# Kernel tuning notes

Hardware: AMD Instinct MI355X
Metric: run time of the kernel (lower is better)

The kernel has to match this reference:

```python
import jax, jax.numpy as jnp
import numpy as np

D_MODEL = 1024
D_STATE = 16
D_CONV = 4
EXPAND = 2
D_INNER = EXPAND * D_MODEL
DT_RANK = (D_MODEL + 15) // 16  # 64
EPS = 1e-5


def dwconv(x, w, b, pad):
    # x: (B, C, L), w: (C, 1, K), depthwise conv
    y = jax.lax.conv_general_dilated(x, w, (1,), [pad],
                                     dimension_numbers=('NCH', 'OIH', 'NCH'),
                                     feature_group_count=x.shape[1])
    return y + b[None, :, None]


def mamba(x, W_inproj, m_conv_w, m_conv_b, W_xproj, W_dt, b_dt, A_log, Dp, W_outproj):
    # x: (B, L, d_model)
    Bn, L, _ = x.shape
    xz = x @ W_inproj.T                       # (B, L, 2*d_inner)
    xi, z = jnp.split(xz, 2, axis=-1)
    # causal depthwise conv: pad (K-1, 0) == torch pad K-1 then slice [:L]
    xc = dwconv(jnp.swapaxes(xi, 1, 2), m_conv_w, m_conv_b, (D_CONV - 1, 0))
    u = jax.nn.silu(jnp.swapaxes(xc, 1, 2))   # (B, L, d_inner)
    x_dbl = u @ W_xproj.T                     # (B, L, dt_rank + 2*d_state)
    dt = x_dbl[..., :DT_RANK]
    Bm = x_dbl[..., DT_RANK:DT_RANK + D_STATE]
    Cm = x_dbl[..., DT_RANK + D_STATE:]
    dt = jax.nn.softplus(dt @ W_dt.T + b_dt)  # (B, L, d_inner)
    A = -jnp.exp(A_log)                       # (d_inner, d_state)

    def step(h, inp):
        dt_t, B_t, C_t, u_t = inp             # (B,di),(B,ds),(B,ds),(B,di)
        dA = jnp.exp(dt_t[..., None] * A)     # (B, di, ds)
        h = dA * h + dt_t[..., None] * B_t[:, None, :] * u_t[..., None]
        y = jnp.einsum('bds,bs->bd', h, C_t)
        return h, y

    tm = lambda a: jnp.swapaxes(a, 0, 1)      # time-major for scan
    h0 = jnp.zeros((Bn, D_INNER, D_STATE), x.dtype)
    _, ys = jax.lax.scan(step, h0, (tm(dt), tm(Bm), tm(Cm), tm(u)))
    y = jnp.swapaxes(ys, 0, 1) + u * Dp       # (B, L, d_inner)
    y = y * jax.nn.silu(z)
    return y @ W_outproj.T                    # (B, L, d_model)


def forward(x, ln_g, ln_b, W_in, b_in, conv_w, conv_b,
            W_inproj, m_conv_w, m_conv_b, W_xproj, W_dt, b_dt,
            A_log, Dp, W_outproj, W_out, b_out):
    h = jnp.swapaxes(x, 1, 2)                 # (B, L, d_model)
    mu = h.mean(-1, keepdims=True)
    var = ((h - mu) ** 2).mean(-1, keepdims=True)
    h = (h - mu) / jnp.sqrt(var + EPS) * ln_g + ln_b
    h = h @ W_in.T + b_in
    # outer depthwise conv: kernel 4, pad 2 each side -> length L+1 (faithful)
    h = dwconv(jnp.swapaxes(h, 1, 2), conv_w, conv_b, (D_CONV // 2, D_CONV // 2))
    h = jax.nn.silu(h)
    h = jnp.swapaxes(h, 1, 2)                 # (B, L+1, d_model)
    y = mamba(h, W_inproj, m_conv_w, m_conv_b, W_xproj, W_dt, b_dt, A_log, Dp, W_outproj)
    y = y @ W_out.T + b_out
    return jnp.swapaxes(y, 1, 2)              # (B, d_model, L+1)


def setup_inputs() -> dict:
    key = jax.random.key(0)
    ks = jax.random.split(key, 16)
    B, L = 2, 2048
    s = 0.02
    inp = {
        'x': jax.random.normal(ks[0], (B, D_MODEL, L), jnp.float32),
        'ln_g': jnp.ones((D_MODEL,), jnp.float32),
        'ln_b': jnp.zeros((D_MODEL,), jnp.float32),
        'W_in': jax.random.normal(ks[1], (D_MODEL, D_MODEL), jnp.float32) * s,
        'b_in': jnp.zeros((D_MODEL,), jnp.float32),
        'conv_w': jax.random.normal(ks[2], (D_MODEL, 1, D_CONV), jnp.float32) * 0.3,
        'conv_b': jnp.zeros((D_MODEL,), jnp.float32),
        'W_inproj': jax.random.normal(ks[3], (2 * D_INNER, D_MODEL), jnp.float32) * s,
        'm_conv_w': jax.random.normal(ks[4], (D_INNER, 1, D_CONV), jnp.float32) * 0.3,
        'm_conv_b': jnp.zeros((D_INNER,), jnp.float32),
        'W_xproj': jax.random.normal(ks[5], (DT_RANK + 2 * D_STATE, D_INNER), jnp.float32) * s,
        'W_dt': jax.random.normal(ks[6], (D_INNER, DT_RANK), jnp.float32) * (DT_RANK ** -0.5),
        'b_dt': jax.random.uniform(ks[7], (D_INNER,), jnp.float32, -4.6, -2.0),
        'A_log': jnp.log(jnp.tile(jnp.arange(1, D_STATE + 1, dtype=jnp.float32)[None, :], (D_INNER, 1))),
        'Dp': jnp.ones((D_INNER,), jnp.float32),
        'W_outproj': jax.random.normal(ks[8], (D_MODEL, D_INNER), jnp.float32) * s,
        'W_out': jax.random.normal(ks[9], (D_MODEL, D_MODEL), jnp.float32) * s,
        'b_out': jnp.zeros((D_MODEL,), jnp.float32),
    }
    return inp


def reference(x, ln_g, ln_b, W_in, b_in, conv_w, conv_b, W_inproj, m_conv_w, m_conv_b,
              W_xproj, W_dt, b_dt, A_log, Dp, W_outproj, W_out, b_out):
    return forward(x, ln_g, ln_b, W_in, b_in, conv_w, conv_b, W_inproj, m_conv_w,
                   m_conv_b, W_xproj, W_dt, b_dt, A_log, Dp, W_outproj, W_out, b_out)
```

## Files before the change

kernel.cpp:

```cpp
#include <hip/hip_runtime.h>
#include <hip/hip_bf16.h>

#define DMODEL 1024
#define DINNER 2048
#define DTRANK 64
#define NPROJ  96
#define BATCH  2
#define LIN    2048
#define LOUT   2049
#define MTOT0  4096
#define MTOT1  4098
#define TC     32
#define NCH    65

typedef __attribute__((ext_vector_type(8))) short short8;
typedef __attribute__((ext_vector_type(4))) float f32x4;

__device__ __forceinline__ float f_silu(float x)     { return x / (1.f + __expf(-x)); }
__device__ __forceinline__ float f_softplus(float x) { return (x > 20.f) ? x : log1pf(__expf(x)); }
__device__ __forceinline__ short f2b(float x)
{
    __hip_bfloat16 b = __float2bfloat16(x);
    return *reinterpret_cast<short*>(&b);
}
__device__ __forceinline__ void gload16(const void* g, void* l)
{
    __builtin_amdgcn_global_load_lds(
        (const __attribute__((address_space(1))) void*)g,
        (__attribute__((address_space(3))) void*)l,
        16, 0, 0);
}
__device__ __forceinline__ void xcd_swizzle(int& bx, int& by)
{
    int nx = gridDim.x;
    int nwg = nx * gridDim.y;
    int f = blockIdx.x + blockIdx.y * nx;
    int xcd = f & 7, i = f >> 3;
    int q = nwg >> 3, r = nwg & 7;
    int w = (xcd < r ? xcd * (q + 1) : r * (q + 1) + (xcd - r) * q) + i;
    bx = w % nx;
    by = w / nx;
}

__global__ void ln_stats_k(const float* __restrict__ x, float* __restrict__ mu, float* __restrict__ rs)
{
    int b  = blockIdx.y;
    int l0 = blockIdx.x * 64;
    int lc = threadIdx.x & 63;
    int q  = threadIdx.x >> 6;
    const float* xb = x + (size_t)b * DMODEL * LIN + (l0 + lc);
    float s = 0.f, ss = 0.f;
    for (int c = q * 256; c < q * 256 + 256; ++c) {
        float v = xb[(size_t)c * LIN];
        s += v; ss += v * v;
    }
    __shared__ float Ss[4][64];
    __shared__ float Sq[4][64];
    Ss[q][lc] = s; Sq[q][lc] = ss;
    __syncthreads();
    if (threadIdx.x < 64) {
        float st = Ss[0][lc] + Ss[1][lc] + Ss[2][lc] + Ss[3][lc];
        float sq = Sq[0][lc] + Sq[1][lc] + Sq[2][lc] + Sq[3][lc];
        float m = st * (1.f / DMODEL);
        float v = sq * (1.f / DMODEL) - m * m;
        mu[b * LIN + l0 + lc] = m;
        rs[b * LIN + l0 + lc] = 1.f / sqrtf(v + 1e-5f);
    }
}

__global__ void lnT_k(const float* __restrict__ x, const float* __restrict__ mu,
                      const float* __restrict__ rs, const float* __restrict__ g,
                      const float* __restrict__ be, short* __restrict__ h0T)
{
    __shared__ float T[32][33];
    int l0 = blockIdx.x * 32;
    int c0 = blockIdx.y * 32;
    int b  = blockIdx.z;
    int tx = threadIdx.x & 31, ty = threadIdx.x >> 5;
    const float* xb = x + ((size_t)b * DMODEL + c0) * LIN + l0;
#pragma unroll
    for (int i = 0; i < 4; i++) {
        int cl = ty + 8 * i;
        T[cl][tx] = xb[(size_t)cl * LIN + tx];
    }
    __syncthreads();
    int c = c0 + tx;
    float gg = g[c], bb = be[c];
#pragma unroll
    for (int i = 0; i < 4; i++) {
        int ll = ty + 8 * i;
        int m = b * LIN + l0 + ll;
        float v = (T[tx][ll] - mu[m]) * rs[m] * gg + bb;
        h0T[(size_t)m * DMODEL + c] = f2b(v);
    }
}

__global__ void wdtT_k(const float* __restrict__ W_dt, float* __restrict__ WdtT)
{
    __shared__ float T[32][33];
    int n0 = blockIdx.x * 32;
    int k0 = blockIdx.y * 32;
    int tx = threadIdx.x & 31, ty = threadIdx.x >> 5;
#pragma unroll
    for (int i = 0; i < 4; i++) {
        int r = ty + 8 * i;
        T[r][tx] = W_dt[(size_t)(n0 + r) * 64 + k0 + tx];
    }
    __syncthreads();
#pragma unroll
    for (int i = 0; i < 4; i++) {
        int r = ty + 8 * i;
        WdtT[(size_t)(k0 + r) * 2048 + n0 + tx] = T[tx][r];
    }
}

__global__ void cvt_all_k(const float* __restrict__ W_in, const float* __restrict__ W_inproj,
                          const float* __restrict__ W_xproj,
                          const float* __restrict__ W_outproj, const float* __restrict__ W_out,
                          short* __restrict__ Wib, short* __restrict__ Winpb,
                          short* __restrict__ Wxpb,
                          short* __restrict__ Wopb, short* __restrict__ Wob)
{
    int b = blockIdx.x;
    const float* s; short* d; int i;
    if      (b < 1024) { s = W_in;      d = Wib;   i = b; }
    else if (b < 5120) { s = W_inproj;  d = Winpb; i = b - 1024; }
    else if (b < 5312) { s = W_xproj;   d = Wxpb;  i = b - 5120; }
    else if (b < 7360) { s = W_outproj; d = Wopb;  i = b - 5312; }
    else               { s = W_out;     d = Wob;   i = b - 7360; }
    int idx = (i * 256 + threadIdx.x) * 4;
    float4 v = *(const float4*)(s + idx);
    d[idx + 0] = f2b(v.x); d[idx + 1] = f2b(v.y);
    d[idx + 2] = f2b(v.z); d[idx + 3] = f2b(v.w);
}

template<int EPI>
__global__ __launch_bounds__(256) void gemm_bf(
    const short* __restrict__ A, int lda,
    const short* __restrict__ W, int ldb,
    float* __restrict__ C, int ldc,
    short* __restrict__ Cb, int ldcb,
    int M, int N, int K,
    const float* __restrict__ bias)
{
    __shared__ char LDSall[16896];
    short* As = (short*)LDSall;
    short* Bs = (short*)(LDSall + 8192);

    int tid  = threadIdx.x;
    int lane = tid & 63, wid = tid >> 6;
    int wr = wid >> 1, wc = wid & 1;
    int fr = lane & 15, kg = lane >> 4;
    int bx, by;
    xcd_swizzle(bx, by);
    int m0 = bx * 128, n0 = by * 128;

    int scol  = (lane & 3) * 8;
    int srow0 = wid * 32 + (lane >> 2);
    int srow1 = srow0 + 16;
    const short* a0 = A + (size_t)(m0 + srow0) * lda + scol;
    const short* a1 = A + (size_t)(m0 + srow1) * lda + scol;
    const short* b0 = W + (size_t)(n0 + srow0) * ldb + scol;
    const short* b1 = W + (size_t)(n0 + srow1) * ldb + scol;
    char* asd0 = LDSall + (wid * 2 + 0) * 1024;
    char* asd1 = LDSall + (wid * 2 + 1) * 1024;
    char* bsd0 = LDSall + 8192 + (wid * 2 + 0) * 1024;
    char* bsd1 = LDSall + 8192 + (wid * 2 + 1) * 1024;

    f32x4 acc[4][4];
#pragma unroll
    for (int mi = 0; mi < 4; mi++)
#pragma unroll
        for (int ni = 0; ni < 4; ni++) acc[mi][ni] = (f32x4){0.f, 0.f, 0.f, 0.f};

    for (int k0 = 0; k0 < K; k0 += 32) {
        gload16(a0 + k0, asd0);
        gload16(a1 + k0, asd1);
        gload16(b0 + k0, bsd0);
        gload16(b1 + k0, bsd1);
        __syncthreads();

        short8 af[4], bf[4];
#pragma unroll
        for (int mi = 0; mi < 4; mi++)
            af[mi] = *(const short8*)&As[(wr * 64 + mi * 16 + fr) * 32 + kg * 8];
#pragma unroll
        for (int ni = 0; ni < 4; ni++)
            bf[ni] = *(const short8*)&Bs[(wc * 64 + ni * 16 + fr) * 32 + kg * 8];
#pragma unroll
        for (int mi = 0; mi < 4; mi++)
#pragma unroll
            for (int ni = 0; ni < 4; ni++)
                acc[mi][ni] = __builtin_amdgcn_mfma_f32_16x16x32_bf16(
                    af[mi], bf[ni], acc[mi][ni], 0, 0, 0);
        __syncthreads();
    }

    float* ctile = (float*)LDSall;
    int row = tid >> 3;
    int cs  = (tid & 7) * 16;
#pragma unroll
    for (int p = 0; p < 4; p++) {
        __syncthreads();
#pragma unroll
        for (int ni = 0; ni < 4; ni++)
#pragma unroll
            for (int r = 0; r < 4; r++)
                ctile[(wr * 16 + kg * 4 + r) * 132 + wc * 64 + ni * 16 + fr] = acc[p][ni][r];
        __syncthreads();
        int mrow = m0 + ((row < 16) ? (p * 16 + row) : (64 + p * 16 + (row - 16)));
        int n = n0 + cs;
        if (mrow >= M || n >= N) continue;
        const float* src = &ctile[row * 132 + cs];
        if (EPI == 5) {
            float bv = bias[mrow];
            if (n + 15 < N && !(n < LOUT && n + 15 >= LOUT)) {
                int bq = (n >= LOUT) ? 1 : 0;
                float* dst = C + ((size_t)bq * DMODEL + mrow) * LOUT + (n - bq * LOUT);
#pragma unroll
                for (int e = 0; e < 4; e++) {
                    f32x4 v = *(const f32x4*)(src + 4 * e);
                    v += bv;
                    *(f32x4*)(dst + 4 * e) = v;
                }
            } else {
                for (int j = 0; j < 16; j++) {
                    int nj = n + j;
                    if (nj < N) {
                        int bq = (nj >= LOUT) ? 1 : 0;
                        C[((size_t)bq * DMODEL + mrow) * LOUT + (nj - bq * LOUT)] = src[j] + bv;
                    }
                }
            }
        } else if (EPI == 4) {
            short8 o0, o1;
#pragma unroll
            for (int e = 0; e < 8; e++) { o0[e] = f2b(src[e]); o1[e] = f2b(src[8 + e]); }
            *(short8*)&Cb[(size_t)mrow * ldcb + n]     = o0;
            *(short8*)&Cb[(size_t)mrow * ldcb + n + 8] = o1;
        } else {
#pragma unroll
            for (int e = 0; e < 4; e++) {
                f32x4 v = *(const f32x4*)(src + 4 * e);
                if (EPI == 1) v += *(const f32x4*)&bias[n + 4 * e];
                *(f32x4*)&C[(size_t)mrow * ldc + n + 4 * e] = v;
            }
        }
    }
}

__global__ __launch_bounds__(256) void dtfuse2_k(const float* __restrict__ xdbl,
                                                 const float* __restrict__ WdtT,
                                                 const float* __restrict__ b_dt,
                                                 float* __restrict__ dtout)
{
    int t  = threadIdx.x;
    int m0 = blockIdx.x * 8;
    __shared__ float dr[8][64];
    {
        int k = t & 63, r = t >> 6;
        int ma = m0 + r, mb = m0 + r + 4;
        dr[r][k]     = (ma < MTOT1) ? xdbl[(size_t)ma * NPROJ + k] : 0.f;
        dr[r + 4][k] = (mb < MTOT1) ? xdbl[(size_t)mb * NPROJ + k] : 0.f;
    }
    __syncthreads();

    int n0 = t * 4;
    f32x4 acc0[8], acc1[8];
#pragma unroll
    for (int mi = 0; mi < 8; mi++) {
        acc0[mi] = (f32x4){0.f, 0.f, 0.f, 0.f};
        acc1[mi] = (f32x4){0.f, 0.f, 0.f, 0.f};
    }

    for (int k = 0; k < 64; k += 4) {
        f32x4 w0[4], w1[4];
#pragma unroll
        for (int e = 0; e < 4; e++) {
            w0[e] = *(const f32x4*)&WdtT[(size_t)(k + e) * 2048 + n0];
            w1[e] = *(const f32x4*)&WdtT[(size_t)(k + e) * 2048 + n0 + 1024];
        }
#pragma unroll
        for (int mi = 0; mi < 8; mi++) {
            f32x4 d = *(const f32x4*)&dr[mi][k];
#pragma unroll
            for (int e = 0; e < 4; e++) {
                acc0[mi] += d[e] * w0[e];
                acc1[mi] += d[e] * w1[e];
            }
        }
    }

    f32x4 b0 = *(const f32x4*)&b_dt[n0];
    f32x4 b1 = *(const f32x4*)&b_dt[n0 + 1024];
#pragma unroll
    for (int mi = 0; mi < 8; mi++) {
        int m = m0 + mi;
        if (m >= MTOT1) continue;
        f32x4 v0, v1;
#pragma unroll
        for (int e = 0; e < 4; e++) {
            v0[e] = f_softplus(acc0[mi][e] + b0[e]);
            v1[e] = f_softplus(acc1[mi][e] + b1[e]);
        }
        *(f32x4*)&dtout[(size_t)m * DINNER + n0]        = v0;
        *(f32x4*)&dtout[(size_t)m * DINNER + n0 + 1024] = v1;
    }
}

__global__ void conv1_k(const float* __restrict__ h1, const float* __restrict__ cw,
                        const float* __restrict__ cb, short* __restrict__ h2b)
{
    int c = blockIdx.x * 256 + threadIdx.x;
    int m = blockIdx.y;
    int b = (m >= LOUT) ? 1 : 0;
    int l = m - b * LOUT;
    float4 wv = ((const float4*)cw)[c];
    const float* w = (const float*)&wv;
    float acc = cb[c];
#pragma unroll
    for (int k = 0; k < 4; k++) {
        int li = l - 2 + k;
        if (li >= 0 && li < LIN)
            acc += h1[((size_t)b * LIN + li) * DMODEL + c] * w[k];
    }
    h2b[(size_t)m * DMODEL + c] = f2b(f_silu(acc));
}

__global__ void conv2_k(const float* __restrict__ xz, const float* __restrict__ cw,
                        const float* __restrict__ cb, float* __restrict__ u,
                        short* __restrict__ ub)
{
    int d = blockIdx.x * 256 + threadIdx.x;
    int m = blockIdx.y;
    int b = (m >= LOUT) ? 1 : 0;
    int l = m - b * LOUT;
    float4 wv = ((const float4*)cw)[d];
    const float* w = (const float*)&wv;
    float acc = cb[d];
#pragma unroll
    for (int k = 0; k < 4; k++) {
        int li = l - 3 + k;
        if (li >= 0)
            acc += xz[((size_t)b * LOUT + li) * (2 * DINNER) + d] * w[k];
    }
    float s = f_silu(acc);
    u [(size_t)m * DINNER + d] = s;
    ub[(size_t)m * DINNER + d] = f2b(s);
}

__global__ void scan1_k(const float* __restrict__ dt, const float* __restrict__ u,
                        const float* __restrict__ xdbl, const float* __restrict__ A_log,
                        float* __restrict__ sP, float* __restrict__ sH)
{
    int d = blockIdx.x * 256 + threadIdx.x;
    int c = blockIdx.y;
    int b = blockIdx.z;
    int t0 = c * TC;
    int tlen = LOUT - t0; if (tlen > TC) tlen = TC;

    float Ad[16], h[16], P[16];
#pragma unroll
    for (int q = 0; q < 4; q++) {
        float4 av = ((const float4*)A_log)[d * 4 + q];
        Ad[q*4+0] = -__expf(av.x); Ad[q*4+1] = -__expf(av.y);
        Ad[q*4+2] = -__expf(av.z); Ad[q*4+3] = -__expf(av.w);
    }
#pragma unroll
    for (int s = 0; s < 16; s++) { h[s] = 0.f; P[s] = 1.f; }

    size_t row0 = (size_t)b * LOUT + t0;
    const float* dtp = dt + row0 * DINNER + d;
    const float* up  = u  + row0 * DINNER + d;
    const float* Bp  = xdbl + row0 * NPROJ + DTRANK;
    for (int t = 0; t < tlen; t++) {
        float dtt = dtp[(size_t)t * DINNER];
        float du  = dtt * up[(size_t)t * DINNER];
        const float* Bt = Bp + (size_t)t * NPROJ;
#pragma unroll
        for (int s = 0; s < 16; s++) {
            float a = __expf(dtt * Ad[s]);
            h[s] = a * h[s] + du * Bt[s];
            P[s] *= a;
        }
    }
    size_t base = ((size_t)(b * NCH + c) * 16) * DINNER + d;
#pragma unroll
    for (int s = 0; s < 16; s++) {
        sP[base + (size_t)s * DINNER] = P[s];
        sH[base + (size_t)s * DINNER] = h[s];
    }
}

__global__ void scan2_k(const float* __restrict__ sP, float* __restrict__ sH)
{
    int gid = blockIdx.x * 256 + threadIdx.x;
    int d = gid & (DINNER - 1);
    int s = (gid >> 11) & 15;
    int b = gid >> 15;
    size_t base = ((size_t)(b * NCH) * 16 + s) * DINNER + d;
    const size_t cstep = (size_t)16 * DINNER;
    float hrun = 0.f;
    for (int c = 0; c < NCH; c++) {
        size_t idx = base + (size_t)c * cstep;
        float Pv = sP[idx], hl = sH[idx];
        sH[idx] = hrun;
        hrun = Pv * hrun + hl;
    }
}

__global__ void scan3_k(const float* __restrict__ dt, const float* __restrict__ u,
                        const float* __restrict__ xdbl, const float* __restrict__ A_log,
                        const float* __restrict__ Dp, const float* __restrict__ xz,
                        const float* __restrict__ sH, short* __restrict__ ymb)
{
    int d = blockIdx.x * 256 + threadIdx.x;
    int c = blockIdx.y;
    int b = blockIdx.z;
    int t0 = c * TC;
    int tlen = LOUT - t0; if (tlen > TC) tlen = TC;

    float Ad[16], h[16];
#pragma unroll
    for (int q = 0; q < 4; q++) {
        float4 av = ((const float4*)A_log)[d * 4 + q];
        Ad[q*4+0] = -__expf(av.x); Ad[q*4+1] = -__expf(av.y);
        Ad[q*4+2] = -__expf(av.z); Ad[q*4+3] = -__expf(av.w);
    }
    size_t sbase = ((size_t)(b * NCH + c) * 16) * DINNER + d;
#pragma unroll
    for (int s = 0; s < 16; s++) h[s] = sH[sbase + (size_t)s * DINNER];

    float Dpd = Dp[d];
    size_t row0 = (size_t)b * LOUT + t0;
    const float* dtp = dt + row0 * DINNER + d;
    const float* up  = u  + row0 * DINNER + d;
    const float* Bp  = xdbl + row0 * NPROJ + DTRANK;
    const float* Cp  = Bp + 16;
    const float* zp  = xz + row0 * (2 * DINNER) + DINNER + d;
    short* yp = ymb + row0 * DINNER + d;
    for (int t = 0; t < tlen; t++) {
        float dtt = dtp[(size_t)t * DINNER];
        float ut  = up[(size_t)t * DINNER];
        float du  = dtt * ut;
        const float* Bt = Bp + (size_t)t * NPROJ;
        const float* Ct = Cp + (size_t)t * NPROJ;
        float y = 0.f;
#pragma unroll
        for (int s = 0; s < 16; s++) {
            float a = __expf(dtt * Ad[s]);
            h[s] = a * h[s] + du * Bt[s];
            y += h[s] * Ct[s];
        }
        float z = zp[(size_t)t * (2 * DINNER)];
        yp[(size_t)t * DINNER] = f2b((y + ut * Dpd) * f_silu(z));
    }
}

extern "C" void kernel_launch(void* const* d_in, const int* in_sizes, int n_in,
                              void* d_out, int out_size, void* d_ws, size_t ws_size,
                              hipStream_t stream)
{
    (void)in_sizes; (void)n_in; (void)out_size; (void)ws_size;
    const float* x        = (const float*)d_in[0];
    const float* ln_g     = (const float*)d_in[1];
    const float* ln_b     = (const float*)d_in[2];
    const float* W_in     = (const float*)d_in[3];
    const float* b_in     = (const float*)d_in[4];
    const float* conv_w   = (const float*)d_in[5];
    const float* conv_b   = (const float*)d_in[6];
    const float* W_inproj = (const float*)d_in[7];
    const float* m_conv_w = (const float*)d_in[8];
    const float* m_conv_b = (const float*)d_in[9];
    const float* W_xproj  = (const float*)d_in[10];
    const float* W_dt     = (const float*)d_in[11];
    const float* b_dt     = (const float*)d_in[12];
    const float* A_log    = (const float*)d_in[13];
    const float* Dp       = (const float*)d_in[14];
    const float* W_outproj= (const float*)d_in[15];
    const float* W_out    = (const float*)d_in[16];
    const float* b_out    = (const float*)d_in[17];
    float* out = (float*)d_out;

    float* F    = (float*)d_ws;
    float* mu   = F;
    float* rs   = F + 4096;
    float* h1   = F + 8192;
    float* xz   = h1 + (size_t)MTOT0 * DMODEL;
    float* uu   = xz + (size_t)MTOT1 * 2 * DINNER;
    float* xdbl = uu + (size_t)MTOT1 * DINNER;
    float* dt   = xdbl + (size_t)MTOT1 * NPROJ;
    float* sP   = dt + (size_t)MTOT1 * DINNER;
    float* sH   = sP + (size_t)BATCH * NCH * 16 * DINNER;
    float* WdtT = sH + (size_t)BATCH * NCH * 16 * DINNER;
    float* fend = WdtT + (size_t)DTRANK * DINNER;

    short* S     = (short*)fend;
    short* h0T   = S;
    short* h2b   = h0T + (size_t)MTOT0 * DMODEL;
    short* ub    = h2b + (size_t)MTOT1 * DMODEL;
    short* Wib   = ub  + (size_t)MTOT1 * DINNER;
    short* Winpb = Wib   + (size_t)DMODEL * DMODEL;
    short* Wxpb  = Winpb + (size_t)(2*DINNER) * DMODEL;
    short* Wopb  = Wxpb  + (size_t)NPROJ * DINNER;
    short* Wob   = Wopb  + (size_t)DMODEL * DINNER;
    short* ymb   = ub;
    short* o1b   = (short*)h1;

    cvt_all_k<<<8384, 256, 0, stream>>>(W_in, W_inproj, W_xproj, W_outproj, W_out,
                                        Wib, Winpb, Wxpb, Wopb, Wob);
    wdtT_k<<<dim3(64, 2), 256, 0, stream>>>(W_dt, WdtT);
    ln_stats_k<<<dim3(32, 2), 256, 0, stream>>>(x, mu, rs);
    lnT_k<<<dim3(64, 32, 2), 256, 0, stream>>>(x, mu, rs, ln_g, ln_b, h0T);
    gemm_bf<1><<<dim3(32, 8), 256, 0, stream>>>(h0T, DMODEL, Wib, DMODEL,
        h1, DMODEL, nullptr, 0, MTOT0, DMODEL, DMODEL, b_in);
    conv1_k<<<dim3(4, MTOT1), 256, 0, stream>>>(h1, conv_w, conv_b, h2b);
    gemm_bf<0><<<dim3(33, 32), 256, 0, stream>>>(h2b, DMODEL, Winpb, DMODEL,
        xz, 2 * DINNER, nullptr, 0, MTOT1, 2 * DINNER, DMODEL, nullptr);
    conv2_k<<<dim3(8, MTOT1), 256, 0, stream>>>(xz, m_conv_w, m_conv_b, uu, ub);
    gemm_bf<0><<<dim3(33, 1), 256, 0, stream>>>(ub, DINNER, Wxpb, DINNER,
        xdbl, NPROJ, nullptr, 0, MTOT1, NPROJ, DINNER, nullptr);
    dtfuse2_k<<<513, 256, 0, stream>>>(xdbl, WdtT, b_dt, dt);
    scan1_k<<<dim3(8, NCH, 2), 256, 0, stream>>>(dt, uu, xdbl, A_log, sP, sH);
    scan2_k<<<dim3(256), 256, 0, stream>>>(sP, sH);
    scan3_k<<<dim3(8, NCH, 2), 256, 0, stream>>>(dt, uu, xdbl, A_log, Dp, xz, sH, ymb);
    gemm_bf<4><<<dim3(33, 8), 256, 0, stream>>>(ymb, DINNER, Wopb, DINNER,
        nullptr, 0, o1b, DMODEL, MTOT1, DMODEL, DINNER, nullptr);
    gemm_bf<5><<<dim3(8, 33), 256, 0, stream>>>(Wob, DMODEL, o1b, DMODEL,
        out, 0, nullptr, 0, DMODEL, MTOT1, DMODEL, b_out);
}
```

Before: 631.6 us.

## Compute dt projection with bf16 MFMA GEMM and double scan chunk length

```diff
diff --git a/kernel.cpp b/kernel.cpp
--- a/kernel.cpp
+++ b/kernel.cpp
@@ -10,8 +10,8 @@
 #define LOUT   2049
 #define MTOT0  4096
 #define MTOT1  4098
-#define TC     32
-#define NCH    65
+#define TC     64
+#define NCH    33
 
 typedef __attribute__((ext_vector_type(8))) short short8;
 typedef __attribute__((ext_vector_type(4))) float f32x4;
@@ -95,30 +95,11 @@
     }
 }
 
-__global__ void wdtT_k(const float* __restrict__ W_dt, float* __restrict__ WdtT)
-{
-    __shared__ float T[32][33];
-    int n0 = blockIdx.x * 32;
-    int k0 = blockIdx.y * 32;
-    int tx = threadIdx.x & 31, ty = threadIdx.x >> 5;
-#pragma unroll
-    for (int i = 0; i < 4; i++) {
-        int r = ty + 8 * i;
-        T[r][tx] = W_dt[(size_t)(n0 + r) * 64 + k0 + tx];
-    }
-    __syncthreads();
-#pragma unroll
-    for (int i = 0; i < 4; i++) {
-        int r = ty + 8 * i;
-        WdtT[(size_t)(k0 + r) * 2048 + n0 + tx] = T[tx][r];
-    }
-}
-
 __global__ void cvt_all_k(const float* __restrict__ W_in, const float* __restrict__ W_inproj,
-                          const float* __restrict__ W_xproj,
+                          const float* __restrict__ W_xproj, const float* __restrict__ W_dt,
                           const float* __restrict__ W_outproj, const float* __restrict__ W_out,
                           short* __restrict__ Wib, short* __restrict__ Winpb,
-                          short* __restrict__ Wxpb,
+                          short* __restrict__ Wxpb, short* __restrict__ Wdtb,
                           short* __restrict__ Wopb, short* __restrict__ Wob)
 {
     int b = blockIdx.x;
@@ -126,8 +107,9 @@
     if      (b < 1024) { s = W_in;      d = Wib;   i = b; }
     else if (b < 5120) { s = W_inproj;  d = Winpb; i = b - 1024; }
     else if (b < 5312) { s = W_xproj;   d = Wxpb;  i = b - 5120; }
-    else if (b < 7360) { s = W_outproj; d = Wopb;  i = b - 5312; }
-    else               { s = W_out;     d = Wob;   i = b - 7360; }
+    else if (b < 5440) { s = W_dt;      d = Wdtb;  i = b - 5312; }
+    else if (b < 7488) { s = W_outproj; d = Wopb;  i = b - 5440; }
+    else               { s = W_out;     d = Wob;   i = b - 7488; }
     int idx = (i * 256 + threadIdx.x) * 4;
     float4 v = *(const float4*)(s + idx);
     d[idx + 0] = f2b(v.x); d[idx + 1] = f2b(v.y);
@@ -243,68 +225,21 @@
             for (int e = 0; e < 4; e++) {
                 f32x4 v = *(const f32x4*)(src + 4 * e);
                 if (EPI == 1) v += *(const f32x4*)&bias[n + 4 * e];
+                if (EPI == 2) {
+                    f32x4 bb = *(const f32x4*)&bias[n + 4 * e];
+#pragma unroll
+                    for (int j = 0; j < 4; j++) v[j] = f_softplus(v[j] + bb[j]);
+                }
                 *(f32x4*)&C[(size_t)mrow * ldc + n + 4 * e] = v;
             }
-        }
-    }
-}
-
-__global__ __launch_bounds__(256) void dtfuse2_k(const float* __restrict__ xdbl,
-                                                 const float* __restrict__ WdtT,
-                                                 const float* __restrict__ b_dt,
-                                                 float* __restrict__ dtout)
-{
-    int t  = threadIdx.x;
-    int m0 = blockIdx.x * 8;
-    __shared__ float dr[8][64];
-    {
-        int k = t & 63, r = t >> 6;
-        int ma = m0 + r, mb = m0 + r + 4;
-        dr[r][k]     = (ma < MTOT1) ? xdbl[(size_t)ma * NPROJ + k] : 0.f;
-        dr[r + 4][k] = (mb < MTOT1) ? xdbl[(size_t)mb * NPROJ + k] : 0.f;
-    }
-    __syncthreads();
-
-    int n0 = t * 4;
-    f32x4 acc0[8], acc1[8];
-#pragma unroll
-    for (int mi = 0; mi < 8; mi++) {
-        acc0[mi] = (f32x4){0.f, 0.f, 0.f, 0.f};
-        acc1[mi] = (f32x4){0.f, 0.f, 0.f, 0.f};
-    }
-
-    for (int k = 0; k < 64; k += 4) {
-        f32x4 w0[4], w1[4];
-#pragma unroll
-        for (int e = 0; e < 4; e++) {
-            w0[e] = *(const f32x4*)&WdtT[(size_t)(k + e) * 2048 + n0];
-            w1[e] = *(const f32x4*)&WdtT[(size_t)(k + e) * 2048 + n0 + 1024];
-        }
-#pragma unroll
-        for (int mi = 0; mi < 8; mi++) {
-            f32x4 d = *(const f32x4*)&dr[mi][k];
-#pragma unroll
-            for (int e = 0; e < 4; e++) {
-                acc0[mi] += d[e] * w0[e];
-                acc1[mi] += d[e] * w1[e];
+            if (EPI == 3 && n < DTRANK) {
+                short8 o0, o1;
+#pragma unroll
+                for (int e = 0; e < 8; e++) { o0[e] = f2b(src[e]); o1[e] = f2b(src[8 + e]); }
+                *(short8*)&Cb[(size_t)mrow * ldcb + n]     = o0;
+                *(short8*)&Cb[(size_t)mrow * ldcb + n + 8] = o1;
             }
         }
-    }
-
-    f32x4 b0 = *(const f32x4*)&b_dt[n0];
-    f32x4 b1 = *(const f32x4*)&b_dt[n0 + 1024];
-#pragma unroll
-    for (int mi = 0; mi < 8; mi++) {
-        int m = m0 + mi;
-        if (m >= MTOT1) continue;
-        f32x4 v0, v1;
-#pragma unroll
-        for (int e = 0; e < 4; e++) {
-            v0[e] = f_softplus(acc0[mi][e] + b0[e]);
-            v1[e] = f_softplus(acc1[mi][e] + b1[e]);
-        }
-        *(f32x4*)&dtout[(size_t)m * DINNER + n0]        = v0;
-        *(f32x4*)&dtout[(size_t)m * DINNER + n0 + 1024] = v1;
     }
 }
 
@@ -492,8 +427,7 @@
     float* dt   = xdbl + (size_t)MTOT1 * NPROJ;
     float* sP   = dt + (size_t)MTOT1 * DINNER;
     float* sH   = sP + (size_t)BATCH * NCH * 16 * DINNER;
-    float* WdtT = sH + (size_t)BATCH * NCH * 16 * DINNER;
-    float* fend = WdtT + (size_t)DTRANK * DINNER;
+    float* fend = sH + (size_t)BATCH * NCH * 16 * DINNER;
 
     short* S     = (short*)fend;
     short* h0T   = S;
@@ -502,14 +436,15 @@
     short* Wib   = ub  + (size_t)MTOT1 * DINNER;
     short* Winpb = Wib   + (size_t)DMODEL * DMODEL;
     short* Wxpb  = Winpb + (size_t)(2*DINNER) * DMODEL;
-    short* Wopb  = Wxpb  + (size_t)NPROJ * DINNER;
+    short* Wdtb  = Wxpb  + (size_t)NPROJ * DINNER;
+    short* Wopb  = Wdtb  + (size_t)DINNER * DTRANK;
     short* Wob   = Wopb  + (size_t)DMODEL * DINNER;
+    short* dtin  = h0T;
     short* ymb   = ub;
     short* o1b   = (short*)h1;
 
-    cvt_all_k<<<8384, 256, 0, stream>>>(W_in, W_inproj, W_xproj, W_outproj, W_out,
-                                        Wib, Winpb, Wxpb, Wopb, Wob);
-    wdtT_k<<<dim3(64, 2), 256, 0, stream>>>(W_dt, WdtT);
+    cvt_all_k<<<8512, 256, 0, stream>>>(W_in, W_inproj, W_xproj, W_dt, W_outproj, W_out,
+                                        Wib, Winpb, Wxpb, Wdtb, Wopb, Wob);
     ln_stats_k<<<dim3(32, 2), 256, 0, stream>>>(x, mu, rs);
     lnT_k<<<dim3(64, 32, 2), 256, 0, stream>>>(x, mu, rs, ln_g, ln_b, h0T);
     gemm_bf<1><<<dim3(32, 8), 256, 0, stream>>>(h0T, DMODEL, Wib, DMODEL,
@@ -518,9 +453,10 @@
     gemm_bf<0><<<dim3(33, 32), 256, 0, stream>>>(h2b, DMODEL, Winpb, DMODEL,
         xz, 2 * DINNER, nullptr, 0, MTOT1, 2 * DINNER, DMODEL, nullptr);
     conv2_k<<<dim3(8, MTOT1), 256, 0, stream>>>(xz, m_conv_w, m_conv_b, uu, ub);
-    gemm_bf<0><<<dim3(33, 1), 256, 0, stream>>>(ub, DINNER, Wxpb, DINNER,
-        xdbl, NPROJ, nullptr, 0, MTOT1, NPROJ, DINNER, nullptr);
-    dtfuse2_k<<<513, 256, 0, stream>>>(xdbl, WdtT, b_dt, dt);
+    gemm_bf<3><<<dim3(33, 1), 256, 0, stream>>>(ub, DINNER, Wxpb, DINNER,
+        xdbl, NPROJ, dtin, DTRANK, MTOT1, NPROJ, DINNER, nullptr);
+    gemm_bf<2><<<dim3(33, 16), 256, 0, stream>>>(dtin, DTRANK, Wdtb, DTRANK,
+        dt, DINNER, nullptr, 0, MTOT1, DINNER, DTRANK, b_dt);
     scan1_k<<<dim3(8, NCH, 2), 256, 0, stream>>>(dt, uu, xdbl, A_log, sP, sH);
     scan2_k<<<dim3(256), 256, 0, stream>>>(sP, sH);
     scan3_k<<<dim3(8, NCH, 2), 256, 0, stream>>>(dt, uu, xdbl, A_log, Dp, xz, sH, ymb);
```

New measurement: 557.7 us. 11.7% less time.
